# Kernel tuning notes

Measured on AMD Instinct MI355X. Metric: run time of the kernel, lower is better.

Reference implementation:

```python
import jax, jax.numpy as jnp
import numpy as np

B, N, DIN, D, NH, NL = 4, 256, 4, 64, 4, 2
DH = D // NH
EPS = 1e-5
SLOPE = 0.01  # torch LeakyReLU default negative_slope


def setup_inputs() -> dict:
    key = jax.random.key(0)
    ks = jax.random.split(key, 16)
    def p(k, shape, s=0.05):
        return jax.random.normal(k, shape, jnp.float32) * s
    return {
        "feature": jax.random.normal(ks[0], (B, N, N, DIN), jnp.float32),
        "W1": p(ks[1], (DIN, D)), "b1": jnp.zeros((D,), jnp.float32),
        "mw": p(ks[2], (NH, D)), "mb": jnp.zeros((NH,), jnp.float32),
        "bn_gamma": jnp.ones((D,), jnp.float32), "bn_beta": jnp.zeros((D,), jnp.float32),
        "Wq": p(ks[3], (NL, D, D)), "bq": jnp.zeros((NL, D), jnp.float32),
        "Wk": p(ks[4], (NL, D, D)), "bk": jnp.zeros((NL, D), jnp.float32),
        "Wv": p(ks[5], (NL, D, D)), "bv": jnp.zeros((NL, D), jnp.float32),
        "Wo": p(ks[6], (NL, D, D)), "bo": jnp.zeros((NL, D), jnp.float32),
        "ln1_g": jnp.ones((NL, D), jnp.float32), "ln1_b": jnp.zeros((NL, D), jnp.float32),
        "Wff1": p(ks[7], (NL, D, 2 * D)), "bff1": jnp.zeros((NL, 2 * D), jnp.float32),
        "Wff2": p(ks[8], (NL, 2 * D, D)), "bff2": jnp.zeros((NL, D), jnp.float32),
        "ln2_g": jnp.ones((NL, D), jnp.float32), "ln2_b": jnp.zeros((NL, D), jnp.float32),
    }


def _leaky(x):
    return jnp.where(x >= 0, x, SLOPE * x)


def _layer_norm(x, g, b):
    m = x.mean(axis=-1, keepdims=True)
    v = x.var(axis=-1, keepdims=True)
    return g * (x - m) / jnp.sqrt(v + EPS) + b


def reference(feature, W1, b1, mw, mb, bn_gamma, bn_beta,
              Wq, bq, Wk, bk, Wv, bv, Wo, bo, ln1_g, ln1_b,
              Wff1, bff1, Wff2, bff2, ln2_g, ln2_b):
    # linear1: (B,N,N,DIN) -> (B,N,N,D)
    feat = feature @ W1 + b1
    # per-head scalar attention score over node pairs: (NH,B,N,N)
    s = jnp.einsum('bijh,nh->nbij', feat, mw) + mb[:, None, None, None]
    w = jnp.exp(_leaky(s))
    w = w / w.sum(axis=3, keepdims=True)  # softmax-like over second node dim j
    # weighted aggregation: sum over i, then mean over heads -> (B,N,D)
    h = jnp.einsum('nbij,bijh->bjh', w, feat) / NH
    # BatchNorm1d over channels D, stats over (B,N) (training-mode, biased var)
    m = h.mean(axis=(0, 1))
    v = h.var(axis=(0, 1))
    x = bn_gamma * (h - m) / jnp.sqrt(v + EPS) + bn_beta  # (B,N,D)
    # standard post-LN TransformerEncoder, NL layers
    scale = 1.0 / np.sqrt(DH).astype(np.float32)
    for l in range(NL):
        q = (x @ Wq[l] + bq[l]).reshape(B, N, NH, DH)
        k = (x @ Wk[l] + bk[l]).reshape(B, N, NH, DH)
        vv = (x @ Wv[l] + bv[l]).reshape(B, N, NH, DH)
        a = jax.nn.softmax(jnp.einsum('bqhd,bkhd->bhqk', q, k) * scale, axis=-1)
        o = jnp.einsum('bhqk,bkhd->bqhd', a, vv).reshape(B, N, D) @ Wo[l] + bo[l]
        x = _layer_norm(x + o, ln1_g[l], ln1_b[l])
        f = jax.nn.relu(x @ Wff1[l] + bff1[l]) @ Wff2[l] + bff2[l]
        x = _layer_norm(x + f, ln2_g[l], ln2_b[l])
    return x
```

## Files before the change

### kernel.cpp

```cpp
#include <hip/hip_runtime.h>
#include <math.h>

#define B 4
#define N 256
#define DIN 4
#define D 64
#define NH 4
#define NL 2
#define DH 16

constexpr float EPS = 1e-5f;
constexpr float SLOPE = 0.01f;

template <int NF4>
__device__ __forceinline__ void stage(float* dst, const float* src, int t) {
    int lane = t & 63, w = t >> 6;
#pragma unroll
    for (int i0 = 0; i0 < NF4; i0 += 512) {
        int base = i0 + w * 64;
        __builtin_amdgcn_global_load_lds(
            (const __attribute__((address_space(1))) void*)(src + 4 * (base + lane)),
            (__attribute__((address_space(3))) void*)(dst + 4 * base),
            16, 0, 0);
    }
}

__global__ void __launch_bounds__(512) k_rowsum(
    const float* __restrict__ feature, const float* __restrict__ W1,
    const float* __restrict__ b1, const float* __restrict__ mw,
    const float* __restrict__ mb, float* __restrict__ rs,
    float* __restrict__ bnacc ) {
    __shared__ float M[16];
    __shared__ float C[4];
    __shared__ float part[32];
    int t = threadIdx.x;
    int lane = t & 63, w = t >> 6;
    int cb = blockIdx.x;
    if (cb == 0 && t < 128) bnacc[t] = 0.f;
    if (t < 16) {
        int n = t >> 2, kk = t & 3;
        float s = 0.f;
        for (int d = 0; d < D; ++d) s += W1[kk * D + d] * mw[n * D + d];
        M[t] = s;
    } else if (t < 20) {
        int n = t - 16;
        float s = mb[n];
        for (int d = 0; d < D; ++d) s += b1[d] * mw[n * D + d];
        C[n] = s;
    }
    __syncthreads();

    int r = w & 3, mh = w >> 2;
    int bi = cb * 4 + r;
    const float4* fb = (const float4*)(feature) + (size_t)bi * N;
    float sn[4] = {0.f, 0.f, 0.f, 0.f};
#pragma unroll
    for (int mm = 0; mm < 2; ++mm) {
        float4 f = fb[lane + 64 * (mh * 2 + mm)];
#pragma unroll
        for (int n = 0; n < 4; ++n) {
            float s = C[n] + f.x * M[n*4+0] + f.y * M[n*4+1] + f.z * M[n*4+2] + f.w * M[n*4+3];
            s = (s >= 0.f) ? s : SLOPE * s;
            sn[n] += __expf(s);
        }
    }
#pragma unroll
    for (int n = 0; n < 4; ++n)
#pragma unroll
        for (int off = 32; off > 0; off >>= 1) sn[n] += __shfl_xor(sn[n], off);
    if (lane == 0) {
#pragma unroll
        for (int n = 0; n < 4; ++n) part[w * 4 + n] = sn[n];
    }
    __syncthreads();
    if (t < 16) {
        int rr = t >> 2, n = t & 3;
        rs[((size_t)(cb * 4 + rr)) * 4 + n] = part[rr * 4 + n] + part[(rr + 4) * 4 + n];
    }
}

__global__ void __launch_bounds__(512) k_aggregate(
    const float* __restrict__ feature, const float* __restrict__ W1,
    const float* __restrict__ b1, const float* __restrict__ mw,
    const float* __restrict__ mb, const float* __restrict__ rs,
    float* __restrict__ h, float* __restrict__ bnacc) {
    __shared__ float M[16];
    __shared__ float C[4];
    __shared__ float part[8][10];
    __shared__ float gacc[20];
    __shared__ float hs[4][D];
    int t = threadIdx.x;
    int lane = t & 63, w = t >> 6;
    int cb = blockIdx.x;
    if (t < 16) {
        int n = t >> 2, kk = t & 3;
        float s = 0.f;
        for (int d = 0; d < D; ++d) s += W1[kk * D + d] * mw[n * D + d];
        M[t] = s;
    } else if (t < 20) {
        int n = t - 16;
        float s = mb[n];
        for (int d = 0; d < D; ++d) s += b1[d] * mw[n * D + d];
        C[n] = s;
    }
    __syncthreads();

    int b = cb >> 6, j0 = (cb & 63) * 4;
    int i = t & 255, jh = t >> 8;
    const float4* fb = (const float4*)(feature) + ((size_t)(b * N + i) * N + j0 + jh * 2);
    float4 f[2];
    f[0] = fb[0];
    f[1] = fb[1];
    float4 r4 = *(const float4*)(rs + (size_t)(b * N + i) * 4);
    float rinv[4] = {1.f / r4.x, 1.f / r4.y, 1.f / r4.z, 1.f / r4.w};
    float acc[2][5];
#pragma unroll
    for (int jj = 0; jj < 2; ++jj) {
        float wbar = 0.f;
#pragma unroll
        for (int n = 0; n < 4; ++n) {
            float s = C[n] + f[jj].x * M[n*4+0] + f[jj].y * M[n*4+1] + f[jj].z * M[n*4+2] + f[jj].w * M[n*4+3];
            s = (s >= 0.f) ? s : SLOPE * s;
            wbar += __expf(s) * rinv[n];
        }
        wbar *= 0.25f;
        acc[jj][0] = wbar * f[jj].x; acc[jj][1] = wbar * f[jj].y;
        acc[jj][2] = wbar * f[jj].z; acc[jj][3] = wbar * f[jj].w;
        acc[jj][4] = wbar;
    }
#pragma unroll
    for (int jj = 0; jj < 2; ++jj)
#pragma unroll
        for (int c = 0; c < 5; ++c)
#pragma unroll
            for (int off = 32; off > 0; off >>= 1) acc[jj][c] += __shfl_xor(acc[jj][c], off);
    if (lane == 0) {
#pragma unroll
        for (int jj = 0; jj < 2; ++jj)
#pragma unroll
            for (int c = 0; c < 5; ++c) part[w][jj * 5 + c] = acc[jj][c];
    }
    __syncthreads();
    if (t < 20) {
        int jj = t / 5, c = t - jj * 5;
        int g = jj >> 1, jjl = jj & 1;
        gacc[t] = part[g*4+0][jjl*5+c] + part[g*4+1][jjl*5+c]
                + part[g*4+2][jjl*5+c] + part[g*4+3][jjl*5+c];
    }
    __syncthreads();
    if (t < 256) {
        float hv = gacc[w * 5 + 4] * b1[lane];
#pragma unroll
        for (int kk = 0; kk < 4; ++kk) hv += gacc[w * 5 + kk] * W1[kk * D + lane];
        h[((size_t)(b * N + j0 + w)) * D + lane] = hv;
        hs[w][lane] = hv;
    }
    __syncthreads();
    if (t < 64) {
        float s = hs[0][lane] + hs[1][lane] + hs[2][lane] + hs[3][lane];
        float sq = hs[0][lane]*hs[0][lane] + hs[1][lane]*hs[1][lane]
                 + hs[2][lane]*hs[2][lane] + hs[3][lane]*hs[3][lane];
        atomicAdd(bnacc + lane, s);
        atomicAdd(bnacc + D + lane, sq);
    }
}

__global__ void __launch_bounds__(512, 2) k_qkv0(
    const float* __restrict__ h, const float* __restrict__ bnacc,
    const float* __restrict__ bn_g, const float* __restrict__ bn_b,
    const float* __restrict__ Wq, const float* __restrict__ bq,
    const float* __restrict__ Wk, const float* __restrict__ bk,
    const float* __restrict__ Wv, const float* __restrict__ bv,
    float* __restrict__ x, float* __restrict__ q,
    float* __restrict__ k, float* __restrict__ v) {
    __shared__ __align__(16) float xsh[4 * D];
    __shared__ __align__(16) float pp[8 * 192];
    __shared__ __align__(16) float WqL[D * D];
    __shared__ __align__(16) float WkL[D * D];
    __shared__ __align__(16) float WvL[D * D];
    int t = threadIdx.x;
    int lane = t & 63, w = t >> 6;
    int tok4 = w & 3, kh = w >> 2;
    int token = blockIdx.x * 4 + tok4;
    int b = token >> 8, n = token & (N - 1);
    int ch = lane;

    stage<D * D / 4>(WqL, Wq, t);
    stage<D * D / 4>(WkL, Wk, t);
    stage<D * D / 4>(WvL, Wv, t);

    float mean = bnacc[ch] * (1.0f / (B * N));
    float var = bnacc[D + ch] * (1.0f / (B * N)) - mean * mean;
    float inv = rsqrtf(var + EPS);
    size_t xi = (size_t)token * D + ch;
    float xv = bn_g[ch] * (h[xi] - mean) * inv + bn_b[ch];
    float bq_r = bq[ch], bk_r = bk[ch], bv_r = bv[ch];
    if (kh == 0) {
        x[xi] = xv;
        xsh[tok4 * D + ch] = xv;
    }
    __syncthreads();

    const float4* xr4 = (const float4*)(xsh + tok4 * D + kh * 32);
    float aq0=0.f, aq1=0.f, ak0=0.f, ak1=0.f, av0=0.f, av1=0.f;
#pragma unroll
    for (int k4 = 0; k4 < 8; ++k4) {
        float4 xx = xr4[k4];
        int kk = kh * 32 + k4 * 4;
        aq0 += xx.x * WqL[(kk+0)*D+ch] + xx.z * WqL[(kk+2)*D+ch];
        aq1 += xx.y * WqL[(kk+1)*D+ch] + xx.w * WqL[(kk+3)*D+ch];
        ak0 += xx.x * WkL[(kk+0)*D+ch] + xx.z * WkL[(kk+2)*D+ch];
        ak1 += xx.y * WkL[(kk+1)*D+ch] + xx.w * WkL[(kk+3)*D+ch];
        av0 += xx.x * WvL[(kk+0)*D+ch] + xx.z * WvL[(kk+2)*D+ch];
        av1 += xx.y * WvL[(kk+1)*D+ch] + xx.w * WvL[(kk+3)*D+ch];
    }
    float* ppw = pp + w * 192;
    ppw[ch] = aq0 + aq1;
    ppw[64 + ch] = ak0 + ak1;
    ppw[128 + ch] = av0 + av1;
    __syncthreads();
    if (kh == 0) {
        int head = ch >> 4, dh = ch & (DH - 1);
        size_t oidx = (((size_t)(b * NH + head)) * N + n) * DH + dh;
        q[oidx] = bq_r + pp[tok4*192 + ch] + pp[(tok4+4)*192 + ch];
        k[oidx] = bk_r + pp[tok4*192 + 64 + ch] + pp[(tok4+4)*192 + 64 + ch];
        v[oidx] = bv_r + pp[tok4*192 + 128 + ch] + pp[(tok4+4)*192 + 128 + ch];
    }
}

__global__ void __launch_bounds__(512, 2) k_layer(
    const float* __restrict__ q, const float* __restrict__ k,
    const float* __restrict__ v,
    const float* __restrict__ Wo, const float* __restrict__ bo,
    const float* __restrict__ ln1g, const float* __restrict__ ln1b,
    const float* __restrict__ Wff1, const float* __restrict__ bff1,
    const float* __restrict__ Wff2, const float* __restrict__ bff2,
    const float* __restrict__ ln2g, const float* __restrict__ ln2b,
    const float* __restrict__ Wqn, const float* __restrict__ bqn,
    const float* __restrict__ Wkn, const float* __restrict__ bkn,
    const float* __restrict__ Wvn, const float* __restrict__ bvn,
    float* __restrict__ qo, float* __restrict__ ko, float* __restrict__ vo,
    float* __restrict__ x) {
    __shared__ __align__(16) float attS[4 * D];
    __shared__ __align__(16) float xs1[4 * D];
    __shared__ __align__(16) float f1s[4 * 2 * D];
    __shared__ __align__(16) float pp[8 * 192];
    __shared__ __align__(16) float attO[2][4 * D];
    __shared__ float attM[2][16];
    __shared__ float attL[2][16];
    __shared__ __align__(16) float WoL[D * D];
    __shared__ __align__(16) float Wff1L[D * 2 * D];
    __shared__ __align__(16) float Wff2L[2 * D * D];
    __shared__ __align__(16) float WqnL[D * D];
    __shared__ __align__(16) float WknL[D * D];
    __shared__ __align__(16) float WvnL[D * D];

    int t = threadIdx.x;
    int lane = t & 63, w = t >> 6;
    int b = blockIdx.x;
    int q0 = blockIdx.y * 4;
    int h_ = w & 3, half = w >> 2;
    int tok4 = w & 3, kh = w >> 2;
    int token = q0 + tok4;
    int ch = lane;

    int bh = b * NH + h_;
    const float* kb = k + ((size_t)bh * N + half * 128) * DH;
    const float* vb = v + ((size_t)bh * N + half * 128) * DH;
    float4 Kr[2][4], Vr[2][4];
#pragma unroll
    for (int j = 0; j < 2; ++j) {
        int key = lane + 64 * j;
#pragma unroll
        for (int c = 0; c < 4; ++c) {
            Kr[j][c] = *(const float4*)(kb + (size_t)key * DH + 4 * c);
            Vr[j][c] = *(const float4*)(vb + (size_t)key * DH + 4 * c);
        }
    }
    float4 qv[4][4];
#pragma unroll
    for (int qq = 0; qq < 4; ++qq) {
        const float4* qp4 = (const float4*)(q + ((size_t)bh * N + q0 + qq) * DH);
#pragma unroll
        for (int c = 0; c < 4; ++c) qv[qq][c] = qp4[c];
    }

    size_t xidx = ((size_t)b * N + token) * D + ch;
    float xv = x[xidx];
    float bo_r = bo[ch], l1g = ln1g[ch], l1b = ln1b[ch];
    float bf1_r = bff1[kh * D + ch];
    float bf2_r = bff2[ch], l2g = ln2g[ch], l2b = ln2b[ch];
    float bq_r = 0.f, bk_r = 0.f, bv_r = 0.f;
    if (Wqn != nullptr) { bq_r = bqn[ch]; bk_r = bkn[ch]; bv_r = bvn[ch]; }

    stage<1024>(WoL, Wo, t);
    stage<2048>(Wff1L, Wff1, t);
    stage<2048>(Wff2L, Wff2, t);
    if (Wqn != nullptr) {
        stage<1024>(WqnL, Wqn, t);
        stage<1024>(WknL, Wkn, t);
        stage<1024>(WvnL, Wvn, t);
    }

#pragma unroll
    for (int qq = 0; qq < 4; ++qq) {
        float s0 = 0.f, s1 = 0.f;
#pragma unroll
        for (int c = 0; c < 4; ++c) {
            s0 += qv[qq][c].x * Kr[0][c].x + qv[qq][c].y * Kr[0][c].y +
                  qv[qq][c].z * Kr[0][c].z + qv[qq][c].w * Kr[0][c].w;
            s1 += qv[qq][c].x * Kr[1][c].x + qv[qq][c].y * Kr[1][c].y +
                  qv[qq][c].z * Kr[1][c].z + qv[qq][c].w * Kr[1][c].w;
        }
        float m = fmaxf(s0, s1);
#pragma unroll
        for (int off = 32; off > 0; off >>= 1) m = fmaxf(m, __shfl_xor(m, off));
        float p0 = __expf((s0 - m) * 0.25f);
        float p1 = __expf((s1 - m) * 0.25f);
        float lsum = p0 + p1;
#pragma unroll
        for (int off = 32; off > 0; off >>= 1) lsum += __shfl_xor(lsum, off);
        float o[DH];
#pragma unroll
        for (int c = 0; c < 4; ++c) {
            o[4*c+0] = p0 * Vr[0][c].x + p1 * Vr[1][c].x;
            o[4*c+1] = p0 * Vr[0][c].y + p1 * Vr[1][c].y;
            o[4*c+2] = p0 * Vr[0][c].z + p1 * Vr[1][c].z;
            o[4*c+3] = p0 * Vr[0][c].w + p1 * Vr[1][c].w;
        }
#pragma unroll
        for (int d = 0; d < DH; ++d) {
#pragma unroll
            for (int off = 32; off > 0; off >>= 1) o[d] += __shfl_xor(o[d], off);
        }
        if (lane == 0) {
#pragma unroll
            for (int d = 0; d < DH; ++d) attO[half][qq * D + h_ * DH + d] = o[d];
            attM[half][qq * 4 + h_] = m;
            attL[half][qq * 4 + h_] = lsum;
        }
    }
    __syncthreads();

    if (w < 4) {
        int qq = w;
        int head = ch >> 4;
        float m0 = attM[0][qq * 4 + head], m1 = attM[1][qq * 4 + head];
        float l0 = attL[0][qq * 4 + head], l1 = attL[1][qq * 4 + head];
        float M = fmaxf(m0, m1);
        float e0 = __expf((m0 - M) * 0.25f);
        float e1 = __expf((m1 - M) * 0.25f);
        float rl = 1.f / (l0 * e0 + l1 * e1);
        attS[qq * D + ch] = (attO[0][qq * D + ch] * e0 + attO[1][qq * D + ch] * e1) * rl;
    }
    __syncthreads();

    float* ppw = pp + w * 192;
    {
        const float4* ar4 = (const float4*)(attS + tok4 * D + kh * 32);
        float a0=0.f, a1=0.f, a2=0.f, a3=0.f;
#pragma unroll
        for (int k4 = 0; k4 < 8; ++k4) {
            float4 av = ar4[k4];
            int kk = kh * 32 + k4 * 4;
            a0 += av.x * WoL[(kk+0)*D+ch];
            a1 += av.y * WoL[(kk+1)*D+ch];
            a2 += av.z * WoL[(kk+2)*D+ch];
            a3 += av.w * WoL[(kk+3)*D+ch];
        }
        ppw[ch] = (a0+a1)+(a2+a3);
    }
    __syncthreads();
    float oo = bo_r + pp[tok4*192 + ch] + pp[(tok4+4)*192 + ch];
    float r = xv + oo;
    float s1 = r, sq1 = r * r;
#pragma unroll
    for (int off = 32; off > 0; off >>= 1) {
        s1 += __shfl_xor(s1, off);
        sq1 += __shfl_xor(sq1, off);
    }
    float mean1 = s1 * (1.0f / D);
    float var1 = sq1 * (1.0f / D) - mean1 * mean1;
    float x1 = l1g * (r - mean1) * rsqrtf(var1 + EPS) + l1b;
    if (kh == 0) xs1[tok4 * D + ch] = x1;
    __syncthreads();

    {
        const float4* xr4 = (const float4*)(xs1 + tok4 * D + kh * 32);
        float u0=0.f,u1=0.f,u2=0.f,u3=0.f, g0=0.f,g1=0.f,g2=0.f,g3=0.f;
#pragma unroll
        for (int k4 = 0; k4 < 8; ++k4) {
            float4 xx = xr4[k4];
            int kk = kh * 32 + k4 * 4;
            u0 += xx.x * Wff1L[(kk+0)*128+ch];
            u1 += xx.y * Wff1L[(kk+1)*128+ch];
            u2 += xx.z * Wff1L[(kk+2)*128+ch];
            u3 += xx.w * Wff1L[(kk+3)*128+ch];
            g0 += xx.x * Wff1L[(kk+0)*128+64+ch];
            g1 += xx.y * Wff1L[(kk+1)*128+64+ch];
            g2 += xx.z * Wff1L[(kk+2)*128+64+ch];
            g3 += xx.w * Wff1L[(kk+3)*128+64+ch];
        }
        ppw[ch] = (u0+u1)+(u2+u3);
        ppw[64+ch] = (g0+g1)+(g2+g3);
    }
    __syncthreads();
    f1s[tok4*128 + kh*64 + ch] =
        fmaxf(pp[tok4*192 + kh*64 + ch] + pp[(tok4+4)*192 + kh*64 + ch] + bf1_r, 0.f);
    __syncthreads();

    {
        const float4* fr4 = (const float4*)(f1s + tok4*128 + kh*64);
        float e0=0.f,e1=0.f,e2=0.f,e3=0.f;
#pragma unroll
        for (int k4 = 0; k4 < 16; ++k4) {
            float4 fv = fr4[k4];
            int kk = kh*64 + k4*4;
            e0 += fv.x * Wff2L[(kk+0)*D+ch];
            e1 += fv.y * Wff2L[(kk+1)*D+ch];
            e2 += fv.z * Wff2L[(kk+2)*D+ch];
            e3 += fv.w * Wff2L[(kk+3)*D+ch];
        }
        ppw[ch] = (e0+e1)+(e2+e3);
    }
    __syncthreads();
    float o2 = bf2_r + pp[tok4*192 + ch] + pp[(tok4+4)*192 + ch];
    float r2 = x1 + o2;
    float s2 = r2, sq2 = r2 * r2;
#pragma unroll
    for (int off = 32; off > 0; off >>= 1) {
        s2 += __shfl_xor(s2, off);
        sq2 += __shfl_xor(sq2, off);
    }
    float mean2 = s2 * (1.0f / D);
    float var2 = sq2 * (1.0f / D) - mean2 * mean2;
    float xnew = l2g * (r2 - mean2) * rsqrtf(var2 + EPS) + l2b;
    if (kh == 0) x[xidx] = xnew;

    if (Wqn != nullptr) {
        if (kh == 0) attS[tok4 * D + ch] = xnew;
        __syncthreads();
        const float4* xr4 = (const float4*)(attS + tok4 * D + kh * 32);
        float aq0=0.f, aq1=0.f, ak0=0.f, ak1=0.f, av0=0.f, av1=0.f;
#pragma unroll
        for (int k4 = 0; k4 < 8; ++k4) {
            float4 xx = xr4[k4];
            int kk = kh * 32 + k4 * 4;
            aq0 += xx.x * WqnL[(kk+0)*D+ch] + xx.z * WqnL[(kk+2)*D+ch];
            aq1 += xx.y * WqnL[(kk+1)*D+ch] + xx.w * WqnL[(kk+3)*D+ch];
            ak0 += xx.x * WknL[(kk+0)*D+ch] + xx.z * WknL[(kk+2)*D+ch];
            ak1 += xx.y * WknL[(kk+1)*D+ch] + xx.w * WknL[(kk+3)*D+ch];
            av0 += xx.x * WvnL[(kk+0)*D+ch] + xx.z * WvnL[(kk+2)*D+ch];
            av1 += xx.y * WvnL[(kk+1)*D+ch] + xx.w * WvnL[(kk+3)*D+ch];
        }
        ppw[ch] = aq0 + aq1;
        ppw[64+ch] = ak0 + ak1;
        ppw[128+ch] = av0 + av1;
        __syncthreads();
        if (kh == 0) {
            int head = ch >> 4, dh = ch & (DH - 1);
            size_t oidx = (((size_t)(b * NH + head)) * N + token) * DH + dh;
            qo[oidx] = bq_r + pp[tok4*192 + ch] + pp[(tok4+4)*192 + ch];
            ko[oidx] = bk_r + pp[tok4*192 + 64 + ch] + pp[(tok4+4)*192 + 64 + ch];
            vo[oidx] = bv_r + pp[tok4*192 + 128 + ch] + pp[(tok4+4)*192 + 128 + ch];
        }
    }
}

extern "C" void kernel_launch(void* const* d_in, const int* in_sizes, int n_in,
                              void* d_out, int out_size, void* d_ws, size_t ws_size,
                              hipStream_t stream) {
    const float* feature = (const float*)d_in[0];
    const float* W1   = (const float*)d_in[1];
    const float* b1   = (const float*)d_in[2];
    const float* mw   = (const float*)d_in[3];
    const float* mb   = (const float*)d_in[4];
    const float* bn_g = (const float*)d_in[5];
    const float* bn_b = (const float*)d_in[6];
    const float* Wq   = (const float*)d_in[7];
    const float* bq   = (const float*)d_in[8];
    const float* Wk   = (const float*)d_in[9];
    const float* bk   = (const float*)d_in[10];
    const float* Wv   = (const float*)d_in[11];
    const float* bv   = (const float*)d_in[12];
    const float* Wo   = (const float*)d_in[13];
    const float* bo   = (const float*)d_in[14];
    const float* ln1g = (const float*)d_in[15];
    const float* ln1b = (const float*)d_in[16];
    const float* Wff1 = (const float*)d_in[17];
    const float* bff1 = (const float*)d_in[18];
    const float* Wff2 = (const float*)d_in[19];
    const float* bff2 = (const float*)d_in[20];
    const float* ln2g = (const float*)d_in[21];
    const float* ln2b = (const float*)d_in[22];

    float* ws    = (float*)d_ws;
    float* rs    = ws;
    float* h     = rs + B * N * NH;
    float* bnacc = h + B * N * D;
    float* q     = bnacc + 128;
    float* k     = q + B * N * D;
    float* v     = k + B * N * D;
    float* x     = (float*)d_out;

    k_rowsum<<<256, 512, 0, stream>>>(feature, W1, b1, mw, mb, rs, bnacc);
    k_aggregate<<<256, 512, 0, stream>>>(feature, W1, b1, mw, mb, rs, h, bnacc);
    k_qkv0<<<256, 512, 0, stream>>>(h, bnacc, bn_g, bn_b,
                                    Wq, bq, Wk, bk, Wv, bv, x, q, k, v);
    k_layer<<<dim3(B, N / 4), 512, 0, stream>>>(q, k, v,
        Wo, bo, ln1g, ln1b, Wff1, bff1, Wff2, bff2, ln2g, ln2b,
        Wq + (size_t)D * D, bq + D, Wk + (size_t)D * D, bk + D,
        Wv + (size_t)D * D, bv + D, q, k, v, x);
    k_layer<<<dim3(B, N / 4), 512, 0, stream>>>(q, k, v,
        Wo + (size_t)D * D, bo + D, ln1g + D, ln1b + D,
        Wff1 + (size_t)D * 2 * D, bff1 + 2 * D,
        Wff2 + (size_t)2 * D * D, bff2 + D, ln2g + D, ln2b + D,
        nullptr, nullptr, nullptr, nullptr, nullptr, nullptr,
        nullptr, nullptr, nullptr, x);
}
```

Before: 156.5 us.

## Fuse all five kernels into one cooperative persistent kernel with grid syncs

Replaces the rowsum, aggregate, qkv0 and two layer kernels with a single cooperative kernel of 256 blocks that uses grid.sync between phases. Weights are staged into LDS once per block and kept there, features and small parameters are prefetched into registers up front, and M/C are computed with wave shuffles instead of serial loops. Queries stay in LDS, and K/V go to double-buffered global arrays, which removes the intermediate h and q buffers. This targets launch gaps and repeated weight staging. In exchange it adds grid-wide barriers and a large LDS footprint that must still let all blocks be co-resident.

```diff
diff --git a/kernel.cpp b/kernel.cpp
--- a/kernel.cpp
+++ b/kernel.cpp
@@ -1,5 +1,8 @@
 #include <hip/hip_runtime.h>
+#include <hip/hip_cooperative_groups.h>
 #include <math.h>
+
+namespace cg = cooperative_groups;
 
 #define B 4
 #define N 256
@@ -25,446 +28,433 @@
     }
 }
 
-__global__ void __launch_bounds__(512) k_rowsum(
+__global__ void __launch_bounds__(512, 2) k_fused(
     const float* __restrict__ feature, const float* __restrict__ W1,
     const float* __restrict__ b1, const float* __restrict__ mw,
-    const float* __restrict__ mb, float* __restrict__ rs,
-    float* __restrict__ bnacc ) {
-    __shared__ float M[16];
-    __shared__ float C[4];
-    __shared__ float part[32];
-    int t = threadIdx.x;
-    int lane = t & 63, w = t >> 6;
-    int cb = blockIdx.x;
-    if (cb == 0 && t < 128) bnacc[t] = 0.f;
-    if (t < 16) {
-        int n = t >> 2, kk = t & 3;
-        float s = 0.f;
-        for (int d = 0; d < D; ++d) s += W1[kk * D + d] * mw[n * D + d];
-        M[t] = s;
-    } else if (t < 20) {
-        int n = t - 16;
-        float s = mb[n];
-        for (int d = 0; d < D; ++d) s += b1[d] * mw[n * D + d];
-        C[n] = s;
-    }
-    __syncthreads();
-
-    int r = w & 3, mh = w >> 2;
-    int bi = cb * 4 + r;
-    const float4* fb = (const float4*)(feature) + (size_t)bi * N;
-    float sn[4] = {0.f, 0.f, 0.f, 0.f};
-#pragma unroll
-    for (int mm = 0; mm < 2; ++mm) {
-        float4 f = fb[lane + 64 * (mh * 2 + mm)];
-#pragma unroll
-        for (int n = 0; n < 4; ++n) {
-            float s = C[n] + f.x * M[n*4+0] + f.y * M[n*4+1] + f.z * M[n*4+2] + f.w * M[n*4+3];
-            s = (s >= 0.f) ? s : SLOPE * s;
-            sn[n] += __expf(s);
-        }
-    }
-#pragma unroll
-    for (int n = 0; n < 4; ++n)
-#pragma unroll
-        for (int off = 32; off > 0; off >>= 1) sn[n] += __shfl_xor(sn[n], off);
-    if (lane == 0) {
-#pragma unroll
-        for (int n = 0; n < 4; ++n) part[w * 4 + n] = sn[n];
-    }
-    __syncthreads();
-    if (t < 16) {
-        int rr = t >> 2, n = t & 3;
-        rs[((size_t)(cb * 4 + rr)) * 4 + n] = part[rr * 4 + n] + part[(rr + 4) * 4 + n];
-    }
-}
-
-__global__ void __launch_bounds__(512) k_aggregate(
-    const float* __restrict__ feature, const float* __restrict__ W1,
-    const float* __restrict__ b1, const float* __restrict__ mw,
-    const float* __restrict__ mb, const float* __restrict__ rs,
-    float* __restrict__ h, float* __restrict__ bnacc) {
-    __shared__ float M[16];
-    __shared__ float C[4];
-    __shared__ float part[8][10];
-    __shared__ float gacc[20];
-    __shared__ float hs[4][D];
-    int t = threadIdx.x;
-    int lane = t & 63, w = t >> 6;
-    int cb = blockIdx.x;
-    if (t < 16) {
-        int n = t >> 2, kk = t & 3;
-        float s = 0.f;
-        for (int d = 0; d < D; ++d) s += W1[kk * D + d] * mw[n * D + d];
-        M[t] = s;
-    } else if (t < 20) {
-        int n = t - 16;
-        float s = mb[n];
-        for (int d = 0; d < D; ++d) s += b1[d] * mw[n * D + d];
-        C[n] = s;
-    }
-    __syncthreads();
-
-    int b = cb >> 6, j0 = (cb & 63) * 4;
-    int i = t & 255, jh = t >> 8;
-    const float4* fb = (const float4*)(feature) + ((size_t)(b * N + i) * N + j0 + jh * 2);
-    float4 f[2];
-    f[0] = fb[0];
-    f[1] = fb[1];
-    float4 r4 = *(const float4*)(rs + (size_t)(b * N + i) * 4);
-    float rinv[4] = {1.f / r4.x, 1.f / r4.y, 1.f / r4.z, 1.f / r4.w};
-    float acc[2][5];
-#pragma unroll
-    for (int jj = 0; jj < 2; ++jj) {
-        float wbar = 0.f;
-#pragma unroll
-        for (int n = 0; n < 4; ++n) {
-            float s = C[n] + f[jj].x * M[n*4+0] + f[jj].y * M[n*4+1] + f[jj].z * M[n*4+2] + f[jj].w * M[n*4+3];
-            s = (s >= 0.f) ? s : SLOPE * s;
-            wbar += __expf(s) * rinv[n];
-        }
-        wbar *= 0.25f;
-        acc[jj][0] = wbar * f[jj].x; acc[jj][1] = wbar * f[jj].y;
-        acc[jj][2] = wbar * f[jj].z; acc[jj][3] = wbar * f[jj].w;
-        acc[jj][4] = wbar;
-    }
-#pragma unroll
-    for (int jj = 0; jj < 2; ++jj)
-#pragma unroll
-        for (int c = 0; c < 5; ++c)
-#pragma unroll
-            for (int off = 32; off > 0; off >>= 1) acc[jj][c] += __shfl_xor(acc[jj][c], off);
-    if (lane == 0) {
-#pragma unroll
-        for (int jj = 0; jj < 2; ++jj)
-#pragma unroll
-            for (int c = 0; c < 5; ++c) part[w][jj * 5 + c] = acc[jj][c];
-    }
-    __syncthreads();
-    if (t < 20) {
-        int jj = t / 5, c = t - jj * 5;
-        int g = jj >> 1, jjl = jj & 1;
-        gacc[t] = part[g*4+0][jjl*5+c] + part[g*4+1][jjl*5+c]
-                + part[g*4+2][jjl*5+c] + part[g*4+3][jjl*5+c];
-    }
-    __syncthreads();
-    if (t < 256) {
-        float hv = gacc[w * 5 + 4] * b1[lane];
-#pragma unroll
-        for (int kk = 0; kk < 4; ++kk) hv += gacc[w * 5 + kk] * W1[kk * D + lane];
-        h[((size_t)(b * N + j0 + w)) * D + lane] = hv;
-        hs[w][lane] = hv;
-    }
-    __syncthreads();
-    if (t < 64) {
-        float s = hs[0][lane] + hs[1][lane] + hs[2][lane] + hs[3][lane];
-        float sq = hs[0][lane]*hs[0][lane] + hs[1][lane]*hs[1][lane]
-                 + hs[2][lane]*hs[2][lane] + hs[3][lane]*hs[3][lane];
-        atomicAdd(bnacc + lane, s);
-        atomicAdd(bnacc + D + lane, sq);
-    }
-}
-
-__global__ void __launch_bounds__(512, 2) k_qkv0(
-    const float* __restrict__ h, const float* __restrict__ bnacc,
-    const float* __restrict__ bn_g, const float* __restrict__ bn_b,
+    const float* __restrict__ mb, const float* __restrict__ bn_g,
+    const float* __restrict__ bn_b,
     const float* __restrict__ Wq, const float* __restrict__ bq,
     const float* __restrict__ Wk, const float* __restrict__ bk,
     const float* __restrict__ Wv, const float* __restrict__ bv,
-    float* __restrict__ x, float* __restrict__ q,
-    float* __restrict__ k, float* __restrict__ v) {
-    __shared__ __align__(16) float xsh[4 * D];
-    __shared__ __align__(16) float pp[8 * 192];
-    __shared__ __align__(16) float WqL[D * D];
-    __shared__ __align__(16) float WkL[D * D];
-    __shared__ __align__(16) float WvL[D * D];
-    int t = threadIdx.x;
-    int lane = t & 63, w = t >> 6;
-    int tok4 = w & 3, kh = w >> 2;
-    int token = blockIdx.x * 4 + tok4;
-    int b = token >> 8, n = token & (N - 1);
-    int ch = lane;
-
-    stage<D * D / 4>(WqL, Wq, t);
-    stage<D * D / 4>(WkL, Wk, t);
-    stage<D * D / 4>(WvL, Wv, t);
-
-    float mean = bnacc[ch] * (1.0f / (B * N));
-    float var = bnacc[D + ch] * (1.0f / (B * N)) - mean * mean;
-    float inv = rsqrtf(var + EPS);
-    size_t xi = (size_t)token * D + ch;
-    float xv = bn_g[ch] * (h[xi] - mean) * inv + bn_b[ch];
-    float bq_r = bq[ch], bk_r = bk[ch], bv_r = bv[ch];
-    if (kh == 0) {
-        x[xi] = xv;
-        xsh[tok4 * D + ch] = xv;
-    }
-    __syncthreads();
-
-    const float4* xr4 = (const float4*)(xsh + tok4 * D + kh * 32);
-    float aq0=0.f, aq1=0.f, ak0=0.f, ak1=0.f, av0=0.f, av1=0.f;
-#pragma unroll
-    for (int k4 = 0; k4 < 8; ++k4) {
-        float4 xx = xr4[k4];
-        int kk = kh * 32 + k4 * 4;
-        aq0 += xx.x * WqL[(kk+0)*D+ch] + xx.z * WqL[(kk+2)*D+ch];
-        aq1 += xx.y * WqL[(kk+1)*D+ch] + xx.w * WqL[(kk+3)*D+ch];
-        ak0 += xx.x * WkL[(kk+0)*D+ch] + xx.z * WkL[(kk+2)*D+ch];
-        ak1 += xx.y * WkL[(kk+1)*D+ch] + xx.w * WkL[(kk+3)*D+ch];
-        av0 += xx.x * WvL[(kk+0)*D+ch] + xx.z * WvL[(kk+2)*D+ch];
-        av1 += xx.y * WvL[(kk+1)*D+ch] + xx.w * WvL[(kk+3)*D+ch];
-    }
-    float* ppw = pp + w * 192;
-    ppw[ch] = aq0 + aq1;
-    ppw[64 + ch] = ak0 + ak1;
-    ppw[128 + ch] = av0 + av1;
-    __syncthreads();
-    if (kh == 0) {
-        int head = ch >> 4, dh = ch & (DH - 1);
-        size_t oidx = (((size_t)(b * NH + head)) * N + n) * DH + dh;
-        q[oidx] = bq_r + pp[tok4*192 + ch] + pp[(tok4+4)*192 + ch];
-        k[oidx] = bk_r + pp[tok4*192 + 64 + ch] + pp[(tok4+4)*192 + 64 + ch];
-        v[oidx] = bv_r + pp[tok4*192 + 128 + ch] + pp[(tok4+4)*192 + 128 + ch];
-    }
-}
-
-__global__ void __launch_bounds__(512, 2) k_layer(
-    const float* __restrict__ q, const float* __restrict__ k,
-    const float* __restrict__ v,
     const float* __restrict__ Wo, const float* __restrict__ bo,
     const float* __restrict__ ln1g, const float* __restrict__ ln1b,
     const float* __restrict__ Wff1, const float* __restrict__ bff1,
     const float* __restrict__ Wff2, const float* __restrict__ bff2,
     const float* __restrict__ ln2g, const float* __restrict__ ln2b,
-    const float* __restrict__ Wqn, const float* __restrict__ bqn,
-    const float* __restrict__ Wkn, const float* __restrict__ bkn,
-    const float* __restrict__ Wvn, const float* __restrict__ bvn,
-    float* __restrict__ qo, float* __restrict__ ko, float* __restrict__ vo,
-    float* __restrict__ x) {
+    float* __restrict__ rs, float* __restrict__ bnacc,
+    float* __restrict__ k0, float* __restrict__ v0,
+    float* __restrict__ k1, float* __restrict__ v1,
+    float* __restrict__ xout)
+{
+    __shared__ __align__(16) float WA[3 * D * D];
+    __shared__ __align__(16) float WC[D * D + 4 * D * D];
+    __shared__ __align__(16) float qsh[4 * D];
     __shared__ __align__(16) float attS[4 * D];
     __shared__ __align__(16) float xs1[4 * D];
     __shared__ __align__(16) float f1s[4 * 2 * D];
     __shared__ __align__(16) float pp[8 * 192];
     __shared__ __align__(16) float attO[2][4 * D];
-    __shared__ float attM[2][16];
-    __shared__ float attL[2][16];
-    __shared__ __align__(16) float WoL[D * D];
-    __shared__ __align__(16) float Wff1L[D * 2 * D];
-    __shared__ __align__(16) float Wff2L[2 * D * D];
-    __shared__ __align__(16) float WqnL[D * D];
-    __shared__ __align__(16) float WknL[D * D];
-    __shared__ __align__(16) float WvnL[D * D];
-
+    __shared__ float attM[2][16], attL[2][16];
+    __shared__ float rsP[32];
+    __shared__ float part[8][10];
+    __shared__ float gacc[20];
+    __shared__ float hsm[4][D];
+
+    cg::grid_group grid = cg::this_grid();
     int t = threadIdx.x;
     int lane = t & 63, w = t >> 6;
-    int b = blockIdx.x;
-    int q0 = blockIdx.y * 4;
-    int h_ = w & 3, half = w >> 2;
-    int tok4 = w & 3, kh = w >> 2;
-    int token = q0 + tok4;
-    int ch = lane;
-
-    int bh = b * NH + h_;
-    const float* kb = k + ((size_t)bh * N + half * 128) * DH;
-    const float* vb = v + ((size_t)bh * N + half * 128) * DH;
-    float4 Kr[2][4], Vr[2][4];
-#pragma unroll
-    for (int j = 0; j < 2; ++j) {
-        int key = lane + 64 * j;
-#pragma unroll
-        for (int c = 0; c < 4; ++c) {
-            Kr[j][c] = *(const float4*)(kb + (size_t)key * DH + 4 * c);
-            Vr[j][c] = *(const float4*)(vb + (size_t)key * DH + 4 * c);
-        }
+    int cb = blockIdx.x;
+    int b = cb >> 6, q0 = (cb & 63) * 4;
+
+    int r_ = w & 3, mh_ = w >> 2;
+    int bi = cb * 4 + r_;
+    const float4* fbP1 = (const float4*)feature + (size_t)bi * N;
+    float4 fP1[2];
+    fP1[0] = fbP1[lane + 64 * (mh_ * 2 + 0)];
+    fP1[1] = fbP1[lane + 64 * (mh_ * 2 + 1)];
+    int iP2 = t & 255, jhP2 = t >> 8;
+    const float4* fbP2 = (const float4*)feature + ((size_t)(b * N + iP2) * N + q0 + jhP2 * 2);
+    float4 fP2[2];
+    fP2[0] = fbP2[0];
+    fP2[1] = fbP2[1];
+    float w1v[4];
+#pragma unroll
+    for (int kk = 0; kk < 4; ++kk) w1v[kk] = W1[kk * D + lane];
+    float b1v = b1[lane];
+    float mwv4[4];
+#pragma unroll
+    for (int n = 0; n < 4; ++n) mwv4[n] = mw[n * D + lane];
+
+    stage<1024>(WA, Wq, t);
+    stage<1024>(WA + 4096, Wk, t);
+    stage<1024>(WA + 8192, Wv, t);
+    stage<1024>(WC, Wo, t);
+    stage<2048>(WC + 4096, Wff1, t);
+    stage<2048>(WC + 12288, Wff2, t);
+
+    if (cb == 0 && t < 128) bnacc[t] = 0.f;
+
+    float Mreg[16], Creg[4];
+#pragma unroll
+    for (int n = 0; n < 4; ++n) {
+        float mwv = mwv4[n];
+        float p0 = w1v[0] * mwv, p1 = w1v[1] * mwv;
+        float p2 = w1v[2] * mwv, p3 = w1v[3] * mwv;
+        float pc = b1v * mwv;
+#pragma unroll
+        for (int off = 32; off > 0; off >>= 1) {
+            p0 += __shfl_xor(p0, off); p1 += __shfl_xor(p1, off);
+            p2 += __shfl_xor(p2, off); p3 += __shfl_xor(p3, off);
+            pc += __shfl_xor(pc, off);
+        }
+        Mreg[n * 4 + 0] = p0; Mreg[n * 4 + 1] = p1;
+        Mreg[n * 4 + 2] = p2; Mreg[n * 4 + 3] = p3;
+        Creg[n] = pc + mb[n];
     }
-    float4 qv[4][4];
-#pragma unroll
-    for (int qq = 0; qq < 4; ++qq) {
-        const float4* qp4 = (const float4*)(q + ((size_t)bh * N + q0 + qq) * DH);
-#pragma unroll
-        for (int c = 0; c < 4; ++c) qv[qq][c] = qp4[c];
+
+    {
+        float sn[4] = {0.f, 0.f, 0.f, 0.f};
+#pragma unroll
+        for (int mm = 0; mm < 2; ++mm) {
+            float4 f = fP1[mm];
+#pragma unroll
+            for (int n = 0; n < 4; ++n) {
+                float s = Creg[n] + f.x * Mreg[n*4+0] + f.y * Mreg[n*4+1]
+                                  + f.z * Mreg[n*4+2] + f.w * Mreg[n*4+3];
+                s = (s >= 0.f) ? s : SLOPE * s;
+                sn[n] += __expf(s);
+            }
+        }
+#pragma unroll
+        for (int n = 0; n < 4; ++n)
+#pragma unroll
+            for (int off = 32; off > 0; off >>= 1) sn[n] += __shfl_xor(sn[n], off);
+        if (lane == 0) {
+#pragma unroll
+            for (int n = 0; n < 4; ++n) rsP[w * 4 + n] = sn[n];
+        }
+        __syncthreads();
+        if (t < 16) {
+            int rr = t >> 2, n = t & 3;
+            rs[(size_t)(cb * 4 + rr) * 4 + n] = rsP[rr * 4 + n] + rsP[(rr + 4) * 4 + n];
+        }
     }
-
-    size_t xidx = ((size_t)b * N + token) * D + ch;
-    float xv = x[xidx];
-    float bo_r = bo[ch], l1g = ln1g[ch], l1b = ln1b[ch];
-    float bf1_r = bff1[kh * D + ch];
-    float bf2_r = bff2[ch], l2g = ln2g[ch], l2b = ln2b[ch];
-    float bq_r = 0.f, bk_r = 0.f, bv_r = 0.f;
-    if (Wqn != nullptr) { bq_r = bqn[ch]; bk_r = bkn[ch]; bv_r = bvn[ch]; }
-
-    stage<1024>(WoL, Wo, t);
-    stage<2048>(Wff1L, Wff1, t);
-    stage<2048>(Wff2L, Wff2, t);
-    if (Wqn != nullptr) {
-        stage<1024>(WqnL, Wqn, t);
-        stage<1024>(WknL, Wkn, t);
-        stage<1024>(WvnL, Wvn, t);
+    __threadfence();
+    grid.sync();
+
+    {
+        float4 r4 = *(const float4*)(rs + (size_t)(b * N + iP2) * 4);
+        float rinv[4] = {1.f / r4.x, 1.f / r4.y, 1.f / r4.z, 1.f / r4.w};
+        float acc[2][5];
+#pragma unroll
+        for (int jj = 0; jj < 2; ++jj) {
+            float wbar = 0.f;
+#pragma unroll
+            for (int n = 0; n < 4; ++n) {
+                float s = Creg[n] + fP2[jj].x * Mreg[n*4+0] + fP2[jj].y * Mreg[n*4+1]
+                                  + fP2[jj].z * Mreg[n*4+2] + fP2[jj].w * Mreg[n*4+3];
+                s = (s >= 0.f) ? s : SLOPE * s;
+                wbar += __expf(s) * rinv[n];
+            }
+            wbar *= 0.25f;
+            acc[jj][0] = wbar * fP2[jj].x; acc[jj][1] = wbar * fP2[jj].y;
+            acc[jj][2] = wbar * fP2[jj].z; acc[jj][3] = wbar * fP2[jj].w;
+            acc[jj][4] = wbar;
+        }
+#pragma unroll
+        for (int jj = 0; jj < 2; ++jj)
+#pragma unroll
+            for (int c = 0; c < 5; ++c)
+#pragma unroll
+                for (int off = 32; off > 0; off >>= 1) acc[jj][c] += __shfl_xor(acc[jj][c], off);
+        if (lane == 0) {
+#pragma unroll
+            for (int jj = 0; jj < 2; ++jj)
+#pragma unroll
+                for (int c = 0; c < 5; ++c) part[w][jj * 5 + c] = acc[jj][c];
+        }
+        __syncthreads();
+        if (t < 20) {
+            int jj = t / 5, c = t - jj * 5;
+            int g = jj >> 1, jjl = jj & 1;
+            gacc[t] = part[g*4+0][jjl*5+c] + part[g*4+1][jjl*5+c]
+                    + part[g*4+2][jjl*5+c] + part[g*4+3][jjl*5+c];
+        }
+        __syncthreads();
+        if (t < 256) {
+            float hv = gacc[w * 5 + 4] * b1v;
+#pragma unroll
+            for (int kk = 0; kk < 4; ++kk) hv += gacc[w * 5 + kk] * w1v[kk];
+            hsm[w][lane] = hv;
+        }
+        __syncthreads();
+        if (t < 64) {
+            float s = hsm[0][lane] + hsm[1][lane] + hsm[2][lane] + hsm[3][lane];
+            float sq = hsm[0][lane]*hsm[0][lane] + hsm[1][lane]*hsm[1][lane]
+                     + hsm[2][lane]*hsm[2][lane] + hsm[3][lane]*hsm[3][lane];
+            atomicAdd(bnacc + lane, s);
+            atomicAdd(bnacc + D + lane, sq);
+        }
     }
-
-#pragma unroll
-    for (int qq = 0; qq < 4; ++qq) {
-        float s0 = 0.f, s1 = 0.f;
-#pragma unroll
-        for (int c = 0; c < 4; ++c) {
-            s0 += qv[qq][c].x * Kr[0][c].x + qv[qq][c].y * Kr[0][c].y +
-                  qv[qq][c].z * Kr[0][c].z + qv[qq][c].w * Kr[0][c].w;
-            s1 += qv[qq][c].x * Kr[1][c].x + qv[qq][c].y * Kr[1][c].y +
-                  qv[qq][c].z * Kr[1][c].z + qv[qq][c].w * Kr[1][c].w;
-        }
-        float m = fmaxf(s0, s1);
-#pragma unroll
-        for (int off = 32; off > 0; off >>= 1) m = fmaxf(m, __shfl_xor(m, off));
-        float p0 = __expf((s0 - m) * 0.25f);
-        float p1 = __expf((s1 - m) * 0.25f);
-        float lsum = p0 + p1;
-#pragma unroll
-        for (int off = 32; off > 0; off >>= 1) lsum += __shfl_xor(lsum, off);
-        float o[DH];
-#pragma unroll
-        for (int c = 0; c < 4; ++c) {
-            o[4*c+0] = p0 * Vr[0][c].x + p1 * Vr[1][c].x;
-            o[4*c+1] = p0 * Vr[0][c].y + p1 * Vr[1][c].y;
-            o[4*c+2] = p0 * Vr[0][c].z + p1 * Vr[1][c].z;
-            o[4*c+3] = p0 * Vr[0][c].w + p1 * Vr[1][c].w;
-        }
-#pragma unroll
-        for (int d = 0; d < DH; ++d) {
-#pragma unroll
-            for (int off = 32; off > 0; off >>= 1) o[d] += __shfl_xor(o[d], off);
-        }
-        if (lane == 0) {
-#pragma unroll
-            for (int d = 0; d < DH; ++d) attO[half][qq * D + h_ * DH + d] = o[d];
-            attM[half][qq * 4 + h_] = m;
-            attL[half][qq * 4 + h_] = lsum;
-        }
-    }
-    __syncthreads();
-
-    if (w < 4) {
-        int qq = w;
-        int head = ch >> 4;
-        float m0 = attM[0][qq * 4 + head], m1 = attM[1][qq * 4 + head];
-        float l0 = attL[0][qq * 4 + head], l1 = attL[1][qq * 4 + head];
-        float M = fmaxf(m0, m1);
-        float e0 = __expf((m0 - M) * 0.25f);
-        float e1 = __expf((m1 - M) * 0.25f);
-        float rl = 1.f / (l0 * e0 + l1 * e1);
-        attS[qq * D + ch] = (attO[0][qq * D + ch] * e0 + attO[1][qq * D + ch] * e1) * rl;
-    }
-    __syncthreads();
-
-    float* ppw = pp + w * 192;
+    __threadfence();
+    grid.sync();
+
+    float xv;
     {
-        const float4* ar4 = (const float4*)(attS + tok4 * D + kh * 32);
-        float a0=0.f, a1=0.f, a2=0.f, a3=0.f;
-#pragma unroll
-        for (int k4 = 0; k4 < 8; ++k4) {
-            float4 av = ar4[k4];
-            int kk = kh * 32 + k4 * 4;
-            a0 += av.x * WoL[(kk+0)*D+ch];
-            a1 += av.y * WoL[(kk+1)*D+ch];
-            a2 += av.z * WoL[(kk+2)*D+ch];
-            a3 += av.w * WoL[(kk+3)*D+ch];
-        }
-        ppw[ch] = (a0+a1)+(a2+a3);
-    }
-    __syncthreads();
-    float oo = bo_r + pp[tok4*192 + ch] + pp[(tok4+4)*192 + ch];
-    float r = xv + oo;
-    float s1 = r, sq1 = r * r;
-#pragma unroll
-    for (int off = 32; off > 0; off >>= 1) {
-        s1 += __shfl_xor(s1, off);
-        sq1 += __shfl_xor(sq1, off);
-    }
-    float mean1 = s1 * (1.0f / D);
-    float var1 = sq1 * (1.0f / D) - mean1 * mean1;
-    float x1 = l1g * (r - mean1) * rsqrtf(var1 + EPS) + l1b;
-    if (kh == 0) xs1[tok4 * D + ch] = x1;
-    __syncthreads();
-
-    {
-        const float4* xr4 = (const float4*)(xs1 + tok4 * D + kh * 32);
-        float u0=0.f,u1=0.f,u2=0.f,u3=0.f, g0=0.f,g1=0.f,g2=0.f,g3=0.f;
+        int tok4 = w & 3, kh = w >> 2;
+        int token = q0 + tok4;
+        int ch = lane;
+        float mean = bnacc[ch] * (1.0f / (B * N));
+        float var = bnacc[D + ch] * (1.0f / (B * N)) - mean * mean;
+        float inv = rsqrtf(var + EPS);
+        float xvv = bn_g[ch] * (hsm[tok4][ch] - mean) * inv + bn_b[ch];
+        xv = xvv;
+        if (kh == 0) attS[tok4 * D + ch] = xvv;
+        __syncthreads();
+        const float4* xr4 = (const float4*)(attS + tok4 * D + kh * 32);
+        float aq0=0.f, aq1=0.f, ak0=0.f, ak1=0.f, av0=0.f, av1=0.f;
 #pragma unroll
         for (int k4 = 0; k4 < 8; ++k4) {
             float4 xx = xr4[k4];
             int kk = kh * 32 + k4 * 4;
-            u0 += xx.x * Wff1L[(kk+0)*128+ch];
-            u1 += xx.y * Wff1L[(kk+1)*128+ch];
-            u2 += xx.z * Wff1L[(kk+2)*128+ch];
-            u3 += xx.w * Wff1L[(kk+3)*128+ch];
-            g0 += xx.x * Wff1L[(kk+0)*128+64+ch];
-            g1 += xx.y * Wff1L[(kk+1)*128+64+ch];
-            g2 += xx.z * Wff1L[(kk+2)*128+64+ch];
-            g3 += xx.w * Wff1L[(kk+3)*128+64+ch];
-        }
-        ppw[ch] = (u0+u1)+(u2+u3);
-        ppw[64+ch] = (g0+g1)+(g2+g3);
-    }
-    __syncthreads();
-    f1s[tok4*128 + kh*64 + ch] =
-        fmaxf(pp[tok4*192 + kh*64 + ch] + pp[(tok4+4)*192 + kh*64 + ch] + bf1_r, 0.f);
-    __syncthreads();
-
-    {
-        const float4* fr4 = (const float4*)(f1s + tok4*128 + kh*64);
-        float e0=0.f,e1=0.f,e2=0.f,e3=0.f;
-#pragma unroll
-        for (int k4 = 0; k4 < 16; ++k4) {
-            float4 fv = fr4[k4];
-            int kk = kh*64 + k4*4;
-            e0 += fv.x * Wff2L[(kk+0)*D+ch];
-            e1 += fv.y * Wff2L[(kk+1)*D+ch];
-            e2 += fv.z * Wff2L[(kk+2)*D+ch];
-            e3 += fv.w * Wff2L[(kk+3)*D+ch];
-        }
-        ppw[ch] = (e0+e1)+(e2+e3);
-    }
-    __syncthreads();
-    float o2 = bf2_r + pp[tok4*192 + ch] + pp[(tok4+4)*192 + ch];
-    float r2 = x1 + o2;
-    float s2 = r2, sq2 = r2 * r2;
-#pragma unroll
-    for (int off = 32; off > 0; off >>= 1) {
-        s2 += __shfl_xor(s2, off);
-        sq2 += __shfl_xor(sq2, off);
-    }
-    float mean2 = s2 * (1.0f / D);
-    float var2 = sq2 * (1.0f / D) - mean2 * mean2;
-    float xnew = l2g * (r2 - mean2) * rsqrtf(var2 + EPS) + l2b;
-    if (kh == 0) x[xidx] = xnew;
-
-    if (Wqn != nullptr) {
-        if (kh == 0) attS[tok4 * D + ch] = xnew;
-        __syncthreads();
-        const float4* xr4 = (const float4*)(attS + tok4 * D + kh * 32);
-        float aq0=0.f, aq1=0.f, ak0=0.f, ak1=0.f, av0=0.f, av1=0.f;
-#pragma unroll
-        for (int k4 = 0; k4 < 8; ++k4) {
-            float4 xx = xr4[k4];
-            int kk = kh * 32 + k4 * 4;
-            aq0 += xx.x * WqnL[(kk+0)*D+ch] + xx.z * WqnL[(kk+2)*D+ch];
-            aq1 += xx.y * WqnL[(kk+1)*D+ch] + xx.w * WqnL[(kk+3)*D+ch];
-            ak0 += xx.x * WknL[(kk+0)*D+ch] + xx.z * WknL[(kk+2)*D+ch];
-            ak1 += xx.y * WknL[(kk+1)*D+ch] + xx.w * WknL[(kk+3)*D+ch];
-            av0 += xx.x * WvnL[(kk+0)*D+ch] + xx.z * WvnL[(kk+2)*D+ch];
-            av1 += xx.y * WvnL[(kk+1)*D+ch] + xx.w * WvnL[(kk+3)*D+ch];
-        }
+            aq0 += xx.x * WA[(kk+0)*D+ch] + xx.z * WA[(kk+2)*D+ch];
+            aq1 += xx.y * WA[(kk+1)*D+ch] + xx.w * WA[(kk+3)*D+ch];
+            ak0 += xx.x * WA[4096+(kk+0)*D+ch] + xx.z * WA[4096+(kk+2)*D+ch];
+            ak1 += xx.y * WA[4096+(kk+1)*D+ch] + xx.w * WA[4096+(kk+3)*D+ch];
+            av0 += xx.x * WA[8192+(kk+0)*D+ch] + xx.z * WA[8192+(kk+2)*D+ch];
+            av1 += xx.y * WA[8192+(kk+1)*D+ch] + xx.w * WA[8192+(kk+3)*D+ch];
+        }
+        float* ppw = pp + w * 192;
         ppw[ch] = aq0 + aq1;
-        ppw[64+ch] = ak0 + ak1;
-        ppw[128+ch] = av0 + av1;
+        ppw[64 + ch] = ak0 + ak1;
+        ppw[128 + ch] = av0 + av1;
         __syncthreads();
         if (kh == 0) {
             int head = ch >> 4, dh = ch & (DH - 1);
-            size_t oidx = (((size_t)(b * NH + head)) * N + token) * DH + dh;
-            qo[oidx] = bq_r + pp[tok4*192 + ch] + pp[(tok4+4)*192 + ch];
-            ko[oidx] = bk_r + pp[tok4*192 + 64 + ch] + pp[(tok4+4)*192 + 64 + ch];
-            vo[oidx] = bv_r + pp[tok4*192 + 128 + ch] + pp[(tok4+4)*192 + 128 + ch];
+            size_t oidx = (((size_t)(b * NH + head)) * N + (token & (N - 1))) * DH + dh;
+            qsh[tok4 * D + ch] = bq[ch] + pp[tok4*192 + ch] + pp[(tok4+4)*192 + ch];
+            k0[oidx] = bk[ch] + pp[tok4*192 + 64 + ch] + pp[(tok4+4)*192 + 64 + ch];
+            v0[oidx] = bv[ch] + pp[tok4*192 + 128 + ch] + pp[(tok4+4)*192 + 128 + ch];
         }
     }
+    __threadfence();
+    grid.sync();
+
+    auto layer = [&](const float* kg, const float* vg,
+                     const float* boP, const float* l1gP, const float* l1bP,
+                     const float* bf1P, const float* bf2P,
+                     const float* l2gP, const float* l2bP,
+                     int stMode, const float* sA, const float* sB, const float* sC,
+                     bool fuse, const float* bqnP, const float* bknP, const float* bvnP,
+                     float* kOut, float* vOut, bool writeX) {
+        int h_ = w & 3, half = w >> 2;
+        int tok4 = h_, kh = half;
+        int token = q0 + tok4;
+        int ch = lane;
+        int bh = b * NH + h_;
+        const float* kb = kg + ((size_t)bh * N + half * 128) * DH;
+        const float* vb = vg + ((size_t)bh * N + half * 128) * DH;
+        float4 Kr[2][4], Vr[2][4];
+#pragma unroll
+        for (int j = 0; j < 2; ++j) {
+            int key = lane + 64 * j;
+#pragma unroll
+            for (int c = 0; c < 4; ++c) {
+                Kr[j][c] = *(const float4*)(kb + (size_t)key * DH + 4 * c);
+                Vr[j][c] = *(const float4*)(vb + (size_t)key * DH + 4 * c);
+            }
+        }
+        float bo_r = boP[ch], l1g = l1gP[ch], l1b = l1bP[ch];
+        float bf1_r = bf1P[kh * D + ch];
+        float bf2_r = bf2P[ch], l2g = l2gP[ch], l2b = l2bP[ch];
+        float bq_r = 0.f, bk_r = 0.f, bv_r = 0.f;
+        if (fuse) { bq_r = bqnP[ch]; bk_r = bknP[ch]; bv_r = bvnP[ch]; }
+
+        if (stMode == 0) {
+            stage<1024>(WA, sA, t);
+            stage<1024>(WA + 4096, sB, t);
+            stage<1024>(WA + 8192, sC, t);
+        } else {
+            stage<1024>(WC, sA, t);
+            stage<2048>(WC + 4096, sB, t);
+            stage<2048>(WC + 12288, sC, t);
+        }
+
+#pragma unroll
+        for (int qq = 0; qq < 4; ++qq) {
+            const float4* qp4 = (const float4*)(qsh + qq * D + h_ * DH);
+            float4 qv[4] = {qp4[0], qp4[1], qp4[2], qp4[3]};
+            float s0 = 0.f, s1 = 0.f;
+#pragma unroll
+            for (int c = 0; c < 4; ++c) {
+                s0 += qv[c].x*Kr[0][c].x + qv[c].y*Kr[0][c].y + qv[c].z*Kr[0][c].z + qv[c].w*Kr[0][c].w;
+                s1 += qv[c].x*Kr[1][c].x + qv[c].y*Kr[1][c].y + qv[c].z*Kr[1][c].z + qv[c].w*Kr[1][c].w;
+            }
+            float m = fmaxf(s0, s1);
+#pragma unroll
+            for (int off = 32; off > 0; off >>= 1) m = fmaxf(m, __shfl_xor(m, off));
+            float p0 = __expf((s0 - m) * 0.25f);
+            float p1 = __expf((s1 - m) * 0.25f);
+            float lsum = p0 + p1;
+#pragma unroll
+            for (int off = 32; off > 0; off >>= 1) lsum += __shfl_xor(lsum, off);
+            float o[DH];
+#pragma unroll
+            for (int c = 0; c < 4; ++c) {
+                o[4*c+0] = p0 * Vr[0][c].x + p1 * Vr[1][c].x;
+                o[4*c+1] = p0 * Vr[0][c].y + p1 * Vr[1][c].y;
+                o[4*c+2] = p0 * Vr[0][c].z + p1 * Vr[1][c].z;
+                o[4*c+3] = p0 * Vr[0][c].w + p1 * Vr[1][c].w;
+            }
+#pragma unroll
+            for (int d = 0; d < DH; ++d)
+#pragma unroll
+                for (int off = 32; off > 0; off >>= 1) o[d] += __shfl_xor(o[d], off);
+            if (lane == 0) {
+#pragma unroll
+                for (int d = 0; d < DH; ++d) attO[half][qq * D + h_ * DH + d] = o[d];
+                attM[half][qq * 4 + h_] = m;
+                attL[half][qq * 4 + h_] = lsum;
+            }
+        }
+        __syncthreads();
+
+        if (w < 4) {
+            int qq = w;
+            int head = ch >> 4;
+            float m0 = attM[0][qq*4+head], m1 = attM[1][qq*4+head];
+            float l0 = attL[0][qq*4+head], l1 = attL[1][qq*4+head];
+            float M = fmaxf(m0, m1);
+            float e0 = __expf((m0 - M) * 0.25f);
+            float e1 = __expf((m1 - M) * 0.25f);
+            float rl = 1.f / (l0 * e0 + l1 * e1);
+            attS[qq * D + ch] = (attO[0][qq*D+ch] * e0 + attO[1][qq*D+ch] * e1) * rl;
+        }
+        __syncthreads();
+
+        float* ppw = pp + w * 192;
+        {
+            const float4* ar4 = (const float4*)(attS + tok4 * D + kh * 32);
+            float a0=0.f, a1=0.f, a2=0.f, a3=0.f;
+#pragma unroll
+            for (int k4 = 0; k4 < 8; ++k4) {
+                float4 av = ar4[k4];
+                int kk = kh * 32 + k4 * 4;
+                a0 += av.x * WC[(kk+0)*D+ch];
+                a1 += av.y * WC[(kk+1)*D+ch];
+                a2 += av.z * WC[(kk+2)*D+ch];
+                a3 += av.w * WC[(kk+3)*D+ch];
+            }
+            ppw[ch] = (a0+a1)+(a2+a3);
+        }
+        __syncthreads();
+        float oo = bo_r + pp[tok4*192 + ch] + pp[(tok4+4)*192 + ch];
+        float r = xv + oo;
+        float s1v = r, sq1 = r * r;
+#pragma unroll
+        for (int off = 32; off > 0; off >>= 1) {
+            s1v += __shfl_xor(s1v, off);
+            sq1 += __shfl_xor(sq1, off);
+        }
+        float mean1 = s1v * (1.0f / D);
+        float var1 = sq1 * (1.0f / D) - mean1 * mean1;
+        float x1 = l1g * (r - mean1) * rsqrtf(var1 + EPS) + l1b;
+        if (kh == 0) xs1[tok4 * D + ch] = x1;
+        __syncthreads();
+
+        {
+            const float4* xr4 = (const float4*)(xs1 + tok4 * D + kh * 32);
+            float u0=0.f,u1=0.f,u2=0.f,u3=0.f, g0=0.f,g1=0.f,g2=0.f,g3=0.f;
+#pragma unroll
+            for (int k4 = 0; k4 < 8; ++k4) {
+                float4 xx = xr4[k4];
+                int kk = kh * 32 + k4 * 4;
+                u0 += xx.x * WC[4096+(kk+0)*128+ch];
+                u1 += xx.y * WC[4096+(kk+1)*128+ch];
+                u2 += xx.z * WC[4096+(kk+2)*128+ch];
+                u3 += xx.w * WC[4096+(kk+3)*128+ch];
+                g0 += xx.x * WC[4096+(kk+0)*128+64+ch];
+                g1 += xx.y * WC[4096+(kk+1)*128+64+ch];
+                g2 += xx.z * WC[4096+(kk+2)*128+64+ch];
+                g3 += xx.w * WC[4096+(kk+3)*128+64+ch];
+            }
+            ppw[ch] = (u0+u1)+(u2+u3);
+            ppw[64+ch] = (g0+g1)+(g2+g3);
+        }
+        __syncthreads();
+        f1s[tok4*128 + kh*64 + ch] =
+            fmaxf(pp[tok4*192 + kh*64 + ch] + pp[(tok4+4)*192 + kh*64 + ch] + bf1_r, 0.f);
+        __syncthreads();
+
+        {
+            const float4* fr4 = (const float4*)(f1s + tok4*128 + kh*64);
+            float e0=0.f,e1=0.f,e2=0.f,e3=0.f;
+#pragma unroll
+            for (int k4 = 0; k4 < 16; ++k4) {
+                float4 fv = fr4[k4];
+                int kk = kh*64 + k4*4;
+                e0 += fv.x * WC[12288+(kk+0)*D+ch];
+                e1 += fv.y * WC[12288+(kk+1)*D+ch];
+                e2 += fv.z * WC[12288+(kk+2)*D+ch];
+                e3 += fv.w * WC[12288+(kk+3)*D+ch];
+            }
+            ppw[ch] = (e0+e1)+(e2+e3);
+        }
+        __syncthreads();
+        float o2 = bf2_r + pp[tok4*192 + ch] + pp[(tok4+4)*192 + ch];
+        float r2 = x1 + o2;
+        float s2 = r2, sq2 = r2 * r2;
+#pragma unroll
+        for (int off = 32; off > 0; off >>= 1) {
+            s2 += __shfl_xor(s2, off);
+            sq2 += __shfl_xor(sq2, off);
+        }
+        float mean2 = s2 * (1.0f / D);
+        float var2 = sq2 * (1.0f / D) - mean2 * mean2;
+        float xnew = l2g * (r2 - mean2) * rsqrtf(var2 + EPS) + l2b;
+        xv = xnew;
+        if (writeX && kh == 0) xout[((size_t)b * N + token) * D + ch] = xnew;
+
+        if (fuse) {
+            if (kh == 0) attS[tok4 * D + ch] = xnew;
+            __syncthreads();
+            const float4* xr4 = (const float4*)(attS + tok4 * D + kh * 32);
+            float aq0=0.f, aq1=0.f, ak0=0.f, ak1=0.f, av0=0.f, av1=0.f;
+#pragma unroll
+            for (int k4 = 0; k4 < 8; ++k4) {
+                float4 xx = xr4[k4];
+                int kk = kh * 32 + k4 * 4;
+                aq0 += xx.x * WA[(kk+0)*D+ch] + xx.z * WA[(kk+2)*D+ch];
+                aq1 += xx.y * WA[(kk+1)*D+ch] + xx.w * WA[(kk+3)*D+ch];
+                ak0 += xx.x * WA[4096+(kk+0)*D+ch] + xx.z * WA[4096+(kk+2)*D+ch];
+                ak1 += xx.y * WA[4096+(kk+1)*D+ch] + xx.w * WA[4096+(kk+3)*D+ch];
+                av0 += xx.x * WA[8192+(kk+0)*D+ch] + xx.z * WA[8192+(kk+2)*D+ch];
+                av1 += xx.y * WA[8192+(kk+1)*D+ch] + xx.w * WA[8192+(kk+3)*D+ch];
+            }
+            ppw[ch] = aq0 + aq1;
+            ppw[64+ch] = ak0 + ak1;
+            ppw[128+ch] = av0 + av1;
+            __syncthreads();
+            if (kh == 0) {
+                int head = ch >> 4, dh = ch & (DH - 1);
+                size_t oidx = (((size_t)(b * NH + head)) * N + (token & (N - 1))) * DH + dh;
+                qsh[tok4 * D + ch] = bq_r + pp[tok4*192 + ch] + pp[(tok4+4)*192 + ch];
+                kOut[oidx] = bk_r + pp[tok4*192 + 64 + ch] + pp[(tok4+4)*192 + 64 + ch];
+                vOut[oidx] = bv_r + pp[tok4*192 + 128 + ch] + pp[(tok4+4)*192 + 128 + ch];
+            }
+        }
+    };
+
+    layer(k0, v0, bo, ln1g, ln1b, bff1, bff2, ln2g, ln2b,
+          0, Wq + D * D, Wk + D * D, Wv + D * D,
+          true, bq + D, bk + D, bv + D, k1, v1, false);
+    __threadfence();
+    grid.sync();
+
+    layer(k1, v1, bo + D, ln1g + D, ln1b + D, bff1 + 2 * D, bff2 + D,
+          ln2g + D, ln2b + D,
+          1, Wo + D * D, Wff1 + 2 * D * D, Wff2 + 2 * D * D,
+          false, nullptr, nullptr, nullptr, nullptr, nullptr, true);
 }
 
 extern "C" void kernel_launch(void* const* d_in, const int* in_sizes, int n_in,
@@ -496,25 +486,23 @@
 
     float* ws    = (float*)d_ws;
     float* rs    = ws;
-    float* h     = rs + B * N * NH;
-    float* bnacc = h + B * N * D;
-    float* q     = bnacc + 128;
-    float* k     = q + B * N * D;
-    float* v     = k + B * N * D;
-    float* x     = (float*)d_out;
-
-    k_rowsum<<<256, 512, 0, stream>>>(feature, W1, b1, mw, mb, rs, bnacc);
-    k_aggregate<<<256, 512, 0, stream>>>(feature, W1, b1, mw, mb, rs, h, bnacc);
-    k_qkv0<<<256, 512, 0, stream>>>(h, bnacc, bn_g, bn_b,
-                                    Wq, bq, Wk, bk, Wv, bv, x, q, k, v);
-    k_layer<<<dim3(B, N / 4), 512, 0, stream>>>(q, k, v,
-        Wo, bo, ln1g, ln1b, Wff1, bff1, Wff2, bff2, ln2g, ln2b,
-        Wq + (size_t)D * D, bq + D, Wk + (size_t)D * D, bk + D,
-        Wv + (size_t)D * D, bv + D, q, k, v, x);
-    k_layer<<<dim3(B, N / 4), 512, 0, stream>>>(q, k, v,
-        Wo + (size_t)D * D, bo + D, ln1g + D, ln1b + D,
-        Wff1 + (size_t)D * 2 * D, bff1 + 2 * D,
-        Wff2 + (size_t)2 * D * D, bff2 + D, ln2g + D, ln2b + D,
-        nullptr, nullptr, nullptr, nullptr, nullptr, nullptr,
-        nullptr, nullptr, nullptr, x);
+    float* bnacc = rs + B * N * NH;
+    float* k0    = bnacc + 128;
+    float* v0    = k0 + B * N * D;
+    float* k1    = v0 + B * N * D;
+    float* v1    = k1 + B * N * D;
+    float* xout  = (float*)d_out;
+
+    void* args[] = {
+        (void*)&feature, (void*)&W1, (void*)&b1, (void*)&mw, (void*)&mb,
+        (void*)&bn_g, (void*)&bn_b,
+        (void*)&Wq, (void*)&bq, (void*)&Wk, (void*)&bk, (void*)&Wv, (void*)&bv,
+        (void*)&Wo, (void*)&bo, (void*)&ln1g, (void*)&ln1b,
+        (void*)&Wff1, (void*)&bff1, (void*)&Wff2, (void*)&bff2,
+        (void*)&ln2g, (void*)&ln2b,
+        (void*)&rs, (void*)&bnacc, (void*)&k0, (void*)&v0, (void*)&k1, (void*)&v1,
+        (void*)&xout
+    };
+    hipLaunchCooperativeKernel((const void*)k_fused, dim3(256), dim3(512),
+                               args, 0, stream);
 }
```

Result: slower. 445.4 us (+184.6%).
